# Kernel tuning notes

Hardware: AMD Instinct MI355X
Metric: run time of the kernel (lower is better)

## Reference

```python
import jax, jax.numpy as jnp
import numpy as np

KERNEL = 7
PAD = (KERNEL - 1) // 2


def setup_inputs() -> dict:
    key = jax.random.key(0)
    k1, k2 = jax.random.split(key)
    x = jax.random.normal(k1, (32, 256, 64, 64), dtype=jnp.float32)
    W = jax.random.normal(k2, (1, 2, KERNEL, KERNEL), dtype=jnp.float32) * 0.1
    return {"x": x, "W": W}


def reference(x, W):
    # channel-wise max and mean pooling -> [B, 2, H, W]
    x_compress = jnp.concatenate(
        [jnp.max(x, axis=1, keepdims=True), jnp.mean(x, axis=1, keepdims=True)],
        axis=1,
    )
    # 2->1 conv, same padding, no bias/bn/relu
    attn = jax.lax.conv_general_dilated(
        x_compress, W,
        window_strides=(1, 1),
        padding=[(PAD, PAD), (PAD, PAD)],
        dimension_numbers=("NCHW", "OIHW", "NCHW"),
    )
    scale = jax.nn.sigmoid(attn)  # [B, 1, H, W]
    return x * scale
```

## Files before the change

kernel.cpp:

```cpp
#include <hip/hip_runtime.h>
#include <math.h>

#define BB 32
#define CC 256
#define HH 64
#define WW 64
#define HWSZ 4096
#define CHW 1048576

__global__ void sg_reduce(const float* __restrict__ x,
                          float* __restrict__ maxp,
                          float* __restrict__ meanp) {
    int bh = blockIdx.x;
    int b  = bh >> 6;
    int h  = bh & 63;
    int w4 = threadIdx.x & 15;
    int cg = threadIdx.x >> 4;

    const float4* base =
        reinterpret_cast<const float4*>(x + (size_t)b * CHW + h * WW) + w4;
    float4 v = base[(size_t)(cg * 16) * 1024];
    float4 mx = v, sm = v;
    #pragma unroll
    for (int cc = 1; cc < 16; ++cc) {
        float4 u = base[(size_t)(cg * 16 + cc) * 1024];
        mx.x = fmaxf(mx.x, u.x); mx.y = fmaxf(mx.y, u.y);
        mx.z = fmaxf(mx.z, u.z); mx.w = fmaxf(mx.w, u.w);
        sm.x += u.x; sm.y += u.y; sm.z += u.z; sm.w += u.w;
    }

    __shared__ float4 lmax[16][16];
    __shared__ float4 lsum[16][16];
    lmax[cg][w4] = mx;
    lsum[cg][w4] = sm;
    __syncthreads();

    if (threadIdx.x < 16) {
        int w = threadIdx.x;
        float4 M = lmax[0][w];
        float4 S = lsum[0][w];
        #pragma unroll
        for (int g = 1; g < 16; ++g) {
            float4 m2 = lmax[g][w];
            float4 s2 = lsum[g][w];
            M.x = fmaxf(M.x, m2.x); M.y = fmaxf(M.y, m2.y);
            M.z = fmaxf(M.z, m2.z); M.w = fmaxf(M.w, m2.w);
            S.x += s2.x; S.y += s2.y; S.z += s2.z; S.w += s2.w;
        }
        reinterpret_cast<float4*>(maxp)[bh * 16 + w] = M;
        float4 mn;
        mn.x = S.x * (1.0f / CC); mn.y = S.y * (1.0f / CC);
        mn.z = S.z * (1.0f / CC); mn.w = S.w * (1.0f / CC);
        reinterpret_cast<float4*>(meanp)[bh * 16 + w] = mn;
    }
}

__global__ void sg_conv(const float* __restrict__ maxp,
                        const float* __restrict__ meanp,
                        const float* __restrict__ Wt,
                        float* __restrict__ scale) {
    __shared__ float w[98];
    int lt = threadIdx.x;
    if (lt < 98) w[lt] = Wt[lt];
    __syncthreads();

    int t = blockIdx.x * blockDim.x + lt;
    int b = t >> 12;
    int s = t & 4095;
    int h = s >> 6;
    int wc = s & 63;
    const float* mb = maxp  + b * HWSZ;
    const float* nb = meanp + b * HWSZ;

    float acc = 0.0f;
    #pragma unroll
    for (int kh = 0; kh < 7; ++kh) {
        int hh = h + kh - 3;
        if ((unsigned)hh >= (unsigned)HH) continue;
        #pragma unroll
        for (int kw = 0; kw < 7; ++kw) {
            int wcol = wc + kw - 3;
            if ((unsigned)wcol >= (unsigned)WW) continue;
            int o = (hh << 6) + wcol;
            acc = fmaf(mb[o], w[kh * 7 + kw],      acc);
            acc = fmaf(nb[o], w[49 + kh * 7 + kw], acc);
        }
    }
    scale[t] = 1.0f / (1.0f + __expf(-acc));
}

__global__ void sg_apply(const float* __restrict__ x,
                         const float* __restrict__ scale,
                         float* __restrict__ out) {
    const int total4 = BB * CHW / 4;
    int stride = gridDim.x * blockDim.x;
    for (int i = blockIdx.x * blockDim.x + threadIdx.x; i < total4; i += stride) {
        float4 v = reinterpret_cast<const float4*>(x)[i];
        int b  = i >> 18;
        int s4 = i & 1023;
        float4 sc = reinterpret_cast<const float4*>(scale)[(b << 10) + s4];
        v.x *= sc.x; v.y *= sc.y; v.z *= sc.z; v.w *= sc.w;
        reinterpret_cast<float4*>(out)[i] = v;
    }
}

extern "C" void kernel_launch(void* const* d_in, const int* in_sizes, int n_in,
                              void* d_out, int out_size, void* d_ws, size_t ws_size,
                              hipStream_t stream) {
    const float* x  = (const float*)d_in[0];
    const float* Wt = (const float*)d_in[1];
    float* out = (float*)d_out;

    float* wsf   = (float*)d_ws;
    float* maxp  = wsf;
    float* meanp = wsf + BB * HWSZ;
    float* scale = wsf + 2 * BB * HWSZ;

    sg_reduce<<<BB * HH, 256, 0, stream>>>(x, maxp, meanp);
    sg_conv<<<(BB * HWSZ) / 256, 256, 0, stream>>>(maxp, meanp, Wt, scale);
    sg_apply<<<2048, 256, 0, stream>>>(x, scale, out);
}
```

Before: 75.19 us.

## Fuse conv and apply into per-row kernel with nontemporal stores

Merges the 7x7 conv/sigmoid kernel into the apply kernel. Each block computes the 64 scale values for one (batch,row) into shared memory and then multiplies that row across all 256 channels. This removes one launch and the round trip of the scale buffer through global memory. Output is written with nontemporal stores to limit cache pollution. The cost is that only 64 of 256 threads do the conv before a barrier, and the access pattern changes from grid-stride to row-strided across channels.

Result: faster. 73.10 us (-2.8%).

```diff
diff --git a/kernel.cpp b/kernel.cpp
--- a/kernel.cpp
+++ b/kernel.cpp
@@ -8,6 +8,8 @@
 #define HWSZ 4096
 #define CHW 1048576
 
+typedef float f4 __attribute__((ext_vector_type(4)));
+
 __global__ void sg_reduce(const float* __restrict__ x,
                           float* __restrict__ maxp,
                           float* __restrict__ meanp) {
@@ -17,90 +19,88 @@
     int w4 = threadIdx.x & 15;
     int cg = threadIdx.x >> 4;
 
-    const float4* base =
-        reinterpret_cast<const float4*>(x + (size_t)b * CHW + h * WW) + w4;
-    float4 v = base[(size_t)(cg * 16) * 1024];
-    float4 mx = v, sm = v;
+    const f4* base =
+        reinterpret_cast<const f4*>(x + (size_t)b * CHW + h * WW) + w4;
+    f4 v = base[(size_t)(cg * 16) * 1024];
+    f4 mx = v, sm = v;
     #pragma unroll
     for (int cc = 1; cc < 16; ++cc) {
-        float4 u = base[(size_t)(cg * 16 + cc) * 1024];
+        f4 u = base[(size_t)(cg * 16 + cc) * 1024];
         mx.x = fmaxf(mx.x, u.x); mx.y = fmaxf(mx.y, u.y);
         mx.z = fmaxf(mx.z, u.z); mx.w = fmaxf(mx.w, u.w);
-        sm.x += u.x; sm.y += u.y; sm.z += u.z; sm.w += u.w;
+        sm += u;
     }
 
-    __shared__ float4 lmax[16][16];
-    __shared__ float4 lsum[16][16];
+    __shared__ f4 lmax[16][16];
+    __shared__ f4 lsum[16][16];
     lmax[cg][w4] = mx;
     lsum[cg][w4] = sm;
     __syncthreads();
 
     if (threadIdx.x < 16) {
         int w = threadIdx.x;
-        float4 M = lmax[0][w];
-        float4 S = lsum[0][w];
+        f4 M = lmax[0][w];
+        f4 S = lsum[0][w];
         #pragma unroll
         for (int g = 1; g < 16; ++g) {
-            float4 m2 = lmax[g][w];
-            float4 s2 = lsum[g][w];
+            f4 m2 = lmax[g][w];
+            S += lsum[g][w];
             M.x = fmaxf(M.x, m2.x); M.y = fmaxf(M.y, m2.y);
             M.z = fmaxf(M.z, m2.z); M.w = fmaxf(M.w, m2.w);
-            S.x += s2.x; S.y += s2.y; S.z += s2.z; S.w += s2.w;
         }
-        reinterpret_cast<float4*>(maxp)[bh * 16 + w] = M;
-        float4 mn;
-        mn.x = S.x * (1.0f / CC); mn.y = S.y * (1.0f / CC);
-        mn.z = S.z * (1.0f / CC); mn.w = S.w * (1.0f / CC);
-        reinterpret_cast<float4*>(meanp)[bh * 16 + w] = mn;
+        reinterpret_cast<f4*>(maxp)[bh * 16 + w] = M;
+        reinterpret_cast<f4*>(meanp)[bh * 16 + w] = S * (1.0f / CC);
     }
 }
 
-__global__ void sg_conv(const float* __restrict__ maxp,
-                        const float* __restrict__ meanp,
-                        const float* __restrict__ Wt,
-                        float* __restrict__ scale) {
-    __shared__ float w[98];
-    int lt = threadIdx.x;
-    if (lt < 98) w[lt] = Wt[lt];
+__global__ void sg_conv_apply(const float* __restrict__ x,
+                              const float* __restrict__ maxp,
+                              const float* __restrict__ meanp,
+                              const float* __restrict__ Wt,
+                              float* __restrict__ out) {
+    __shared__ float sscale[WW];
+    int bh = blockIdx.x;
+    int b  = bh >> 6;
+    int h  = bh & 63;
+    int tid = threadIdx.x;
+
+    if (tid < WW) {
+        int wc = tid;
+        const float* mb = maxp  + b * HWSZ;
+        const float* nb = meanp + b * HWSZ;
+        float acc = 0.0f;
+        #pragma unroll
+        for (int kh = 0; kh < 7; ++kh) {
+            int hh = h + kh - 3;
+            if ((unsigned)hh >= (unsigned)HH) continue;
+            #pragma unroll
+            for (int kw = 0; kw < 7; ++kw) {
+                int wcol = wc + kw - 3;
+                if ((unsigned)wcol >= (unsigned)WW) continue;
+                int o = (hh << 6) + wcol;
+                acc = fmaf(mb[o], Wt[kh * 7 + kw],      acc);
+                acc = fmaf(nb[o], Wt[49 + kh * 7 + kw], acc);
+            }
+        }
+        sscale[wc] = 1.0f / (1.0f + __expf(-acc));
+    }
     __syncthreads();
 
-    int t = blockIdx.x * blockDim.x + lt;
-    int b = t >> 12;
-    int s = t & 4095;
-    int h = s >> 6;
-    int wc = s & 63;
-    const float* mb = maxp  + b * HWSZ;
-    const float* nb = meanp + b * HWSZ;
+    int w4 = tid & 15;
+    int cg = tid >> 4;
+    f4 sc = reinterpret_cast<const f4*>(sscale)[w4];
 
-    float acc = 0.0f;
+    const f4* xb =
+        reinterpret_cast<const f4*>(x + (size_t)b * CHW + h * WW) + w4;
+    f4* ob =
+        reinterpret_cast<f4*>(out + (size_t)b * CHW + h * WW) + w4;
+
     #pragma unroll
-    for (int kh = 0; kh < 7; ++kh) {
-        int hh = h + kh - 3;
-        if ((unsigned)hh >= (unsigned)HH) continue;
-        #pragma unroll
-        for (int kw = 0; kw < 7; ++kw) {
-            int wcol = wc + kw - 3;
-            if ((unsigned)wcol >= (unsigned)WW) continue;
-            int o = (hh << 6) + wcol;
-            acc = fmaf(mb[o], w[kh * 7 + kw],      acc);
-            acc = fmaf(nb[o], w[49 + kh * 7 + kw], acc);
-        }
-    }
-    scale[t] = 1.0f / (1.0f + __expf(-acc));
-}
-
-__global__ void sg_apply(const float* __restrict__ x,
-                         const float* __restrict__ scale,
-                         float* __restrict__ out) {
-    const int total4 = BB * CHW / 4;
-    int stride = gridDim.x * blockDim.x;
-    for (int i = blockIdx.x * blockDim.x + threadIdx.x; i < total4; i += stride) {
-        float4 v = reinterpret_cast<const float4*>(x)[i];
-        int b  = i >> 18;
-        int s4 = i & 1023;
-        float4 sc = reinterpret_cast<const float4*>(scale)[(b << 10) + s4];
-        v.x *= sc.x; v.y *= sc.y; v.z *= sc.z; v.w *= sc.w;
-        reinterpret_cast<float4*>(out)[i] = v;
+    for (int cc = 0; cc < 16; ++cc) {
+        size_t off = (size_t)(cg * 16 + cc) * 1024;
+        f4 v = xb[off];
+        v *= sc;
+        __builtin_nontemporal_store(v, ob + off);
     }
 }
 
@@ -114,9 +114,7 @@
     float* wsf   = (float*)d_ws;
     float* maxp  = wsf;
     float* meanp = wsf + BB * HWSZ;
-    float* scale = wsf + 2 * BB * HWSZ;
 
     sg_reduce<<<BB * HH, 256, 0, stream>>>(x, maxp, meanp);
-    sg_conv<<<(BB * HWSZ) / 256, 256, 0, stream>>>(maxp, meanp, Wt, scale);
-    sg_apply<<<2048, 256, 0, stream>>>(x, scale, out);
+    sg_conv_apply<<<BB * HH, 256, 0, stream>>>(x, maxp, meanp, Wt, out);
 }
```
